# Performance work log

Measured on AMD Instinct MI355X. Metric: run time of the kernel, lower is better.

Reference implementation:

```python
import jax, jax.numpy as jnp
import numpy as np

N_EMBD = 1024
N_HEAD = 16
B, T = 4, 2048
EPS = 1e-5


def setup_inputs() -> dict:
    key = jax.random.key(0)
    ks = jax.random.split(key, 12)
    s = 0.02
    d, dff = N_EMBD, 4 * N_EMBD
    return {
        "x": jax.random.normal(ks[0], (B, T, d), dtype=jnp.float32),
        "ln1_w": jnp.ones((d,), jnp.float32),
        "ln1_b": jnp.zeros((d,), jnp.float32),
        "ln2_w": jnp.ones((d,), jnp.float32),
        "ln2_b": jnp.zeros((d,), jnp.float32),
        "w_attn": jax.random.normal(ks[1], (d, 3 * d), jnp.float32) * s,
        "b_attn": jnp.zeros((3 * d,), jnp.float32),
        "w_proj": jax.random.normal(ks[2], (d, d), jnp.float32) * s,
        "b_proj": jnp.zeros((d,), jnp.float32),
        "w_fc": jax.random.normal(ks[3], (d, dff), jnp.float32) * s,
        "b_fc": jnp.zeros((dff,), jnp.float32),
        "w_fc2": jax.random.normal(ks[4], (dff, d), jnp.float32) * s,
        "b_fc2": jnp.zeros((d,), jnp.float32),
    }


def _layernorm(x, w, b):
    mu = jnp.mean(x, axis=-1, keepdims=True)
    var = jnp.mean(jnp.square(x - mu), axis=-1, keepdims=True)
    return (x - mu) * jax.lax.rsqrt(var + EPS) * w + b


def reference(x, ln1_w, ln1_b, ln2_w, ln2_b, w_attn, b_attn, w_proj, b_proj,
              w_fc, b_fc, w_fc2, b_fc2):
    Bx, Tx, C = x.shape
    hd = C // N_HEAD
    # --- attention branch ---
    h = _layernorm(x, ln1_w, ln1_b)
    qkv = h @ w_attn + b_attn  # [B,T,3C]
    q, k, v = jnp.split(qkv, 3, axis=-1)
    q = q.reshape(Bx, Tx, N_HEAD, hd).transpose(0, 2, 1, 3)  # [B,H,T,hd]
    k = k.reshape(Bx, Tx, N_HEAD, hd).transpose(0, 2, 1, 3)
    v = v.reshape(Bx, Tx, N_HEAD, hd).transpose(0, 2, 1, 3)
    att = jnp.einsum("bhqd,bhkd->bhqk", q, k) * (1.0 / np.sqrt(hd))
    causal = jnp.tril(jnp.ones((Tx, Tx), dtype=bool))
    att = jnp.where(causal[None, None], att, -jnp.inf)
    att = jax.nn.softmax(att, axis=-1)
    y = jnp.einsum("bhqk,bhkd->bhqd", att, v)
    y = y.transpose(0, 2, 1, 3).reshape(Bx, Tx, C)
    x = x + (y @ w_proj + b_proj)
    # --- mlp branch ---
    h2 = _layernorm(x, ln2_w, ln2_b)
    m = jax.nn.gelu(h2 @ w_fc + b_fc, approximate=False)
    x = x + (m @ w_fc2 + b_fc2)
    return x
```

## Files before the change

### kernel.cpp

```cpp
#include <hip/hip_runtime.h>
#include <hip/hip_bf16.h>
#include <math.h>

typedef __bf16 bf16;
typedef __bf16 bf16x8 __attribute__((ext_vector_type(8)));
typedef float f32x4 __attribute__((ext_vector_type(4)));

__device__ __forceinline__ void gload_lds16(const bf16* g, bf16* l) {
  __builtin_amdgcn_global_load_lds(
      (const __attribute__((address_space(1))) void*)g,
      (__attribute__((address_space(3))) void*)l, 16, 0, 0);
}

#define MF(a, b, c) __builtin_amdgcn_mfma_f32_16x16x32_bf16((a), (b), (c), 0, 0, 0)
#define VM4_BAR()  asm volatile("s_waitcnt vmcnt(4)\ns_barrier" ::: "memory")
#define VM2_BAR()  asm volatile("s_waitcnt vmcnt(2)\ns_barrier" ::: "memory")
#define VM0_BAR()  asm volatile("s_waitcnt vmcnt(0)\ns_barrier" ::: "memory")
#define BAR_ONLY() asm volatile("s_barrier" ::: "memory")
#define LGK0_SB()  do { asm volatile("s_waitcnt lgkmcnt(0)" ::: "memory"); \
                        __builtin_amdgcn_sched_barrier(0); } while (0)

template <int EPI, int KSPLIT>
__global__ __launch_bounds__(512, 2)
void gemmq(const bf16* __restrict__ A, const bf16* __restrict__ BT,
           const float* __restrict__ bias, const float* __restrict__ res,
           void* __restrict__ Cout, void* __restrict__ Cout2,
           int M, int N, int K)
{
  __shared__ alignas(16) bf16 lsA[2][16384];
  __shared__ alignas(16) bf16 lsB[2][16384];

  int nbn = N >> 8;
  int nwg = (M >> 8) * nbn;
  int bid = blockIdx.x;
  int ks = 0;
  if (KSPLIT == 2) { ks = (bid >= nwg) ? 1 : 0; bid -= ks * nwg; }
  int cpx = nwg >> 3;
  int wg  = (bid & 7) * cpx + (bid >> 3);
  int m0 = (wg / nbn) << 8;
  int n0 = (wg % nbn) << 8;

  int t = threadIdx.x;
  int l = t & 63, w = t >> 6;
  int wr = (w >> 2) << 6;
  int wc = (w & 3) << 5;
  int lr = l & 15, lg = l >> 4;

  int kb0 = (KSPLIT == 2) ? ks * (K >> 1) : 0;
  int nt = (K / KSPLIT) >> 6;

  const bf16* Ag = A  + (size_t)m0 * K + kb0;
  const bf16* Bg = BT + (size_t)n0 * K + kb0;

  int swz0 = (lg ^ (lr & 7)) << 3;
  int swz1 = swz0 ^ 32;
  int aRow = (wr + lr) << 6;
  int bRow = (wc + lr) << 6;

  const bf16* srcA[2]; const bf16* srcB[2];
#pragma unroll
  for (int j = 0; j < 2; ++j) {
    int ci = j * 512 + t;
    int r = ci >> 3;
    int g = (ci & 7) ^ (r & 7);
    srcA[j] = Ag + (size_t)r * K + g * 8;
    srcB[j] = Bg + (size_t)r * K + g * 8;
  }
  size_t qA = (size_t)128 * K;

#define STAGE_A(q, kofs, db) do { \
  _Pragma("unroll") \
  for (int j = 0; j < 2; ++j) \
    gload_lds16(srcA[j] + (q) * qA + (kofs), &lsA[db][(q) * 8192 + (j * 512 + t) * 8]); \
} while (0)
#define STAGE_B(q, kofs, db) do { \
  _Pragma("unroll") \
  for (int j = 0; j < 2; ++j) \
    gload_lds16(srcB[j] + (q) * qA + (kofs), &lsB[db][(q) * 8192 + (j * 512 + t) * 8]); \
} while (0)

  f32x4 acc[2][2][4][2];
  f32x4 zero = {0.f, 0.f, 0.f, 0.f};
#pragma unroll
  for (int qa = 0; qa < 2; ++qa)
#pragma unroll
    for (int qb = 0; qb < 2; ++qb)
#pragma unroll
      for (int mi = 0; mi < 4; ++mi)
#pragma unroll
        for (int ni = 0; ni < 2; ++ni) acc[qa][qb][mi][ni] = zero;

  STAGE_A(0, 0, 0);
  STAGE_B(0, 0, 0);
  STAGE_B(1, 0, 0);
  STAGE_A(1, 0, 0);

  bf16x8 afr[4][2], bfr[2][2];

  for (int T = 0; T < nt; ++T) {
    int c = T & 1, d = c ^ 1;
    bool st = (T + 1 < nt);
    int k64 = (T + 1) << 6;
    const bf16* pa = &lsA[c][0];
    const bf16* pb = &lsB[c][0];

    VM4_BAR();
#pragma unroll
    for (int mi = 0; mi < 4; ++mi) {
      afr[mi][0] = *(const bf16x8*)(pa + aRow + mi * 1024 + swz0);
      afr[mi][1] = *(const bf16x8*)(pa + aRow + mi * 1024 + swz1);
    }
#pragma unroll
    for (int ni = 0; ni < 2; ++ni) {
      bfr[ni][0] = *(const bf16x8*)(pb + bRow + ni * 1024 + swz0);
      bfr[ni][1] = *(const bf16x8*)(pb + bRow + ni * 1024 + swz1);
    }
    if (st) STAGE_A(0, k64, d);
    LGK0_SB();
    __builtin_amdgcn_s_setprio(1);
#pragma unroll
    for (int mi = 0; mi < 4; ++mi)
#pragma unroll
      for (int ni = 0; ni < 2; ++ni)
#pragma unroll
        for (int kk = 0; kk < 2; ++kk)
          acc[0][0][mi][ni] = MF(afr[mi][kk], bfr[ni][kk], acc[0][0][mi][ni]);
    __builtin_amdgcn_s_setprio(0);

    if (st) VM4_BAR(); else VM2_BAR();
#pragma unroll
    for (int ni = 0; ni < 2; ++ni) {
      bfr[ni][0] = *(const bf16x8*)(pb + 8192 + bRow + ni * 1024 + swz0);
      bfr[ni][1] = *(const bf16x8*)(pb + 8192 + bRow + ni * 1024 + swz1);
    }
    if (st) STAGE_B(0, k64, d);
    LGK0_SB();
    __builtin_amdgcn_s_setprio(1);
#pragma unroll
    for (int mi = 0; mi < 4; ++mi)
#pragma unroll
      for (int ni = 0; ni < 2; ++ni)
#pragma unroll
        for (int kk = 0; kk < 2; ++kk)
          acc[0][1][mi][ni] = MF(afr[mi][kk], bfr[ni][kk], acc[0][1][mi][ni]);
    __builtin_amdgcn_s_setprio(0);

    if (st) VM4_BAR(); else VM0_BAR();
#pragma unroll
    for (int mi = 0; mi < 4; ++mi) {
      afr[mi][0] = *(const bf16x8*)(pa + 8192 + aRow + mi * 1024 + swz0);
      afr[mi][1] = *(const bf16x8*)(pa + 8192 + aRow + mi * 1024 + swz1);
    }
    if (st) STAGE_B(1, k64, d);
    LGK0_SB();
    __builtin_amdgcn_s_setprio(1);
#pragma unroll
    for (int mi = 0; mi < 4; ++mi)
#pragma unroll
      for (int ni = 0; ni < 2; ++ni)
#pragma unroll
        for (int kk = 0; kk < 2; ++kk)
          acc[1][1][mi][ni] = MF(afr[mi][kk], bfr[ni][kk], acc[1][1][mi][ni]);
    __builtin_amdgcn_s_setprio(0);

    BAR_ONLY();
#pragma unroll
    for (int ni = 0; ni < 2; ++ni) {
      bfr[ni][0] = *(const bf16x8*)(pb + bRow + ni * 1024 + swz0);
      bfr[ni][1] = *(const bf16x8*)(pb + bRow + ni * 1024 + swz1);
    }
    if (st) STAGE_A(1, k64, d);
    LGK0_SB();
    __builtin_amdgcn_s_setprio(1);
#pragma unroll
    for (int mi = 0; mi < 4; ++mi)
#pragma unroll
      for (int ni = 0; ni < 2; ++ni)
#pragma unroll
        for (int kk = 0; kk < 2; ++kk)
          acc[1][0][mi][ni] = MF(afr[mi][kk], bfr[ni][kk], acc[1][0][mi][ni]);
    __builtin_amdgcn_s_setprio(0);
  }

  bf16* Pb = (bf16*)((KSPLIT == 2 && ks) ? Cout2 : Cout);
#pragma unroll
  for (int qa = 0; qa < 2; ++qa)
#pragma unroll
    for (int mi = 0; mi < 4; ++mi) {
      int row = m0 + qa * 128 + wr + mi * 16 + lg * 4;
#pragma unroll
      for (int qb = 0; qb < 2; ++qb)
#pragma unroll
        for (int ni = 0; ni < 2; ++ni) {
          int col = n0 + qb * 128 + wc + ni * 16 + lr;
          float bv = (EPI == 3) ? 0.f : bias[col];
          f32x4 a = acc[qa][qb][mi][ni];
#pragma unroll
          for (int r = 0; r < 4; ++r) {
            float v = a[r] + bv;
            size_t idx = (size_t)(row + r) * N + col;
            if (EPI == 0)      Pb[idx] = (bf16)v;
            else if (EPI == 1) ((float*)Cout)[idx] = v + res[idx];
            else if (EPI == 2) Pb[idx] = (bf16)(0.5f * v * (1.f + erff(v * 0.70710678118654752f)));
            else               Pb[idx] = (bf16)v;
          }
        }
    }
#undef STAGE_A
#undef STAGE_B
}

__global__ __launch_bounds__(256)
void combine2(const bf16* __restrict__ p0, const bf16* __restrict__ p1,
              const float* __restrict__ bias, const float* __restrict__ res,
              float* __restrict__ out)
{
  int i = (blockIdx.x * 256 + threadIdx.x) * 8;
  bf16x8 a = *(const bf16x8*)(p0 + i);
  bf16x8 b = *(const bf16x8*)(p1 + i);
  int c = i & 1023;
#pragma unroll
  for (int j = 0; j < 8; ++j)
    out[i + j] = (float)a[j] + (float)b[j] + bias[c + j] + res[i + j];
}

__global__ __launch_bounds__(256)
void ln_bf16(const float* __restrict__ x, const float* __restrict__ w,
             const float* __restrict__ b, bf16* __restrict__ out)
{
  int row = blockIdx.x;
  int t = threadIdx.x;
  float4 v = ((const float4*)(x + (size_t)row * 1024))[t];
  float s  = v.x + v.y + v.z + v.w;
  float sq = v.x * v.x + v.y * v.y + v.z * v.z + v.w * v.w;
#pragma unroll
  for (int off = 32; off >= 1; off >>= 1) {
    s  += __shfl_xor(s, off);
    sq += __shfl_xor(sq, off);
  }
  __shared__ float ps[4], pq[4];
  if ((t & 63) == 0) { ps[t >> 6] = s; pq[t >> 6] = sq; }
  __syncthreads();
  s  = ps[0] + ps[1] + ps[2] + ps[3];
  sq = pq[0] + pq[1] + pq[2] + pq[3];
  float mu  = s * (1.f / 1024.f);
  float var = sq * (1.f / 1024.f) - mu * mu;
  float rstd = rsqrtf(var + 1e-5f);
  float4 wv = ((const float4*)w)[t];
  float4 bv = ((const float4*)b)[t];
  size_t o0 = (size_t)row * 1024 + t * 4;
  out[o0 + 0] = (bf16)((v.x - mu) * rstd * wv.x + bv.x);
  out[o0 + 1] = (bf16)((v.y - mu) * rstd * wv.y + bv.y);
  out[o0 + 2] = (bf16)((v.z - mu) * rstd * wv.z + bv.z);
  out[o0 + 3] = (bf16)((v.w - mu) * rstd * wv.w + bv.w);
}

__global__ __launch_bounds__(256)
void transpose_cast(const float* __restrict__ W, bf16* __restrict__ WT, int K, int N)
{
  __shared__ float tile[32][33];
  int bk = blockIdx.x * 32, bn = blockIdx.y * 32;
  int tx = threadIdx.x & 31, ty = threadIdx.x >> 5;
#pragma unroll
  for (int i = ty; i < 32; i += 8)
    tile[i][tx] = W[(size_t)(bk + i) * N + bn + tx];
  __syncthreads();
#pragma unroll
  for (int i = ty; i < 32; i += 8)
    WT[(size_t)(bn + i) * K + bk + tx] = (bf16)tile[tx][i];
}

__global__ __launch_bounds__(256)
void vtrans(const bf16* __restrict__ qkv, bf16* __restrict__ vt)
{
  __shared__ alignas(16) bf16 tile[64 * 64];
  int bh = blockIdx.x;
  int b = bh >> 4, h = bh & 15;
  int t0 = blockIdx.y * 64;
  int t = threadIdx.x;
#pragma unroll
  for (int i = 0; i < 2; ++i) {
    int c = i * 256 + t;
    int tt = c >> 3, d8 = c & 7;
    bf16x8 v = *(const bf16x8*)(qkv + (size_t)(b * 2048 + t0 + tt) * 3072 + 2048 + h * 64 + d8 * 8);
    *(bf16x8*)&tile[(tt * 8 + (d8 ^ (tt >> 3))) * 8] = v;
  }
  __syncthreads();
#pragma unroll
  for (int i = 0; i < 2; ++i) {
    int c = i * 256 + t;
    int d = c >> 3, tt8 = c & 7;
    bf16x8 o;
#pragma unroll
    for (int j = 0; j < 8; ++j) {
      int row = tt8 * 8 + j;
      o[j] = tile[(row * 8 + ((d >> 3) ^ (row >> 3))) * 8 + (d & 7)];
    }
    *(bf16x8*)(vt + (size_t)(bh * 64 + d) * 2048 + t0 + tt8 * 8) = o;
  }
}

__global__ __launch_bounds__(256)
void attn_flash(const bf16* __restrict__ qkv, const bf16* __restrict__ vt,
                bf16* __restrict__ y)
{
  __shared__ alignas(16) bf16 lk[64 * 64];
  __shared__ alignas(16) bf16 lv[64 * 64];
  __shared__ alignas(16) bf16 lp[4][16 * 64];

  int bid = blockIdx.x;
  int bh = bid & 63;
  int qb = 31 - (bid >> 6);
  int b = bh >> 4, h = bh & 15;
  int t = threadIdx.x;
  int w = t >> 6, l = t & 63;
  int lr = l & 15, lg = l >> 4;
  int q0 = qb * 64;
  int qw = q0 + w * 16;
  const size_t RS = 3072;
  const float SCL = 0.18033688011112042f;

  const bf16* qbase = qkv + (size_t)(b * 2048) * RS + h * 64;
  const bf16* kbase = qkv + (size_t)(b * 2048) * RS + 1024 + h * 64;
  const bf16* vtb   = vt + (size_t)(bh * 64) * 2048;

  bf16x8 qf[2];
#pragma unroll
  for (int kk = 0; kk < 2; ++kk)
    qf[kk] = *(const bf16x8*)(qbase + (size_t)(qw + lr) * RS + kk * 32 + lg * 8);

  f32x4 zero = {0.f, 0.f, 0.f, 0.f};
  f32x4 o[4];
#pragma unroll
  for (int ni = 0; ni < 4; ++ni) o[ni] = zero;
  float lo[4] = {0.f, 0.f, 0.f, 0.f};

  int nkb = qb + 1;
  for (int kb = 0; kb < nkb; ++kb) {
    int k0 = kb * 64;
#pragma unroll
    for (int i = 0; i < 2; ++i) {
      int c = i * 256 + t;
      int row = c >> 3, c8 = c & 7;
      int sc8 = c8 ^ (row & 7);
      gload_lds16(kbase + (size_t)(k0 + row) * RS + sc8 * 8, &lk[c * 8]);
      gload_lds16(vtb + (size_t)row * 2048 + k0 + sc8 * 8, &lv[c * 8]);
    }
    __syncthreads();

    f32x4 s[4];
#pragma unroll
    for (int j = 0; j < 4; ++j) s[j] = zero;
#pragma unroll
    for (int kk = 0; kk < 2; ++kk)
#pragma unroll
      for (int j = 0; j < 4; ++j) {
        int krow = j * 16 + lr;
        bf16x8 kf = *(const bf16x8*)&lk[krow * 64 + (((4 * kk + lg) ^ (krow & 7)) * 8)];
        s[j] = MF(qf[kk], kf, s[j]);
      }

    bool needmask = (kb == qb);
    float p[4][4];
#pragma unroll
    for (int r = 0; r < 4; ++r) {
      int tq = qw + lg * 4 + r;
#pragma unroll
      for (int j = 0; j < 4; ++j) {
        float v = s[j][r] * SCL;
        if (needmask && (k0 + j * 16 + lr > tq)) v = -1e30f;
        p[j][r] = exp2f(v);
      }
      lo[r] += (p[0][r] + p[1][r]) + (p[2][r] + p[3][r]);
    }

#pragma unroll
    for (int r = 0; r < 4; ++r) {
      int qr = lg * 4 + r;
#pragma unroll
      for (int j = 0; j < 4; ++j) {
        int ch = (2 * j + (lr >> 3)) ^ (qr & 7);
        lp[w][qr * 64 + ch * 8 + (lr & 7)] = (bf16)p[j][r];
      }
    }
    bf16x8 pa[2];
#pragma unroll
    for (int kf = 0; kf < 2; ++kf)
      pa[kf] = *(const bf16x8*)&lp[w][lr * 64 + (((4 * kf + lg) ^ (lr & 7)) * 8)];

#pragma unroll
    for (int ni = 0; ni < 4; ++ni)
#pragma unroll
      for (int kf = 0; kf < 2; ++kf) {
        int d = ni * 16 + lr;
        bf16x8 vf = *(const bf16x8*)&lv[d * 64 + (((4 * kf + lg) ^ (d & 7)) * 8)];
        o[ni] = MF(pa[kf], vf, o[ni]);
      }
    __syncthreads();
  }

#pragma unroll
  for (int r = 0; r < 4; ++r) {
#pragma unroll
    for (int off = 1; off < 16; off <<= 1) lo[r] += __shfl_xor(lo[r], off);
    lo[r] = 1.f / lo[r];
  }
#pragma unroll
  for (int ni = 0; ni < 4; ++ni)
#pragma unroll
    for (int r = 0; r < 4; ++r) {
      int tq = qw + lg * 4 + r;
      y[(size_t)(b * 2048 + tq) * 1024 + h * 64 + ni * 16 + lr] = (bf16)(o[ni][r] * lo[r]);
    }
}

extern "C" void kernel_launch(void* const* d_in, const int* in_sizes, int n_in,
                              void* d_out, int out_size, void* d_ws, size_t ws_size,
                              hipStream_t stream) {
  (void)in_sizes; (void)n_in; (void)out_size; (void)ws_size;
  const float* x      = (const float*)d_in[0];
  const float* ln1w   = (const float*)d_in[1];
  const float* ln1b   = (const float*)d_in[2];
  const float* ln2w   = (const float*)d_in[3];
  const float* ln2b   = (const float*)d_in[4];
  const float* w_attn = (const float*)d_in[5];
  const float* b_attn = (const float*)d_in[6];
  const float* w_proj = (const float*)d_in[7];
  const float* b_proj = (const float*)d_in[8];
  const float* w_fc   = (const float*)d_in[9];
  const float* b_fc   = (const float*)d_in[10];
  const float* w_fc2  = (const float*)d_in[11];
  const float* b_fc2  = (const float*)d_in[12];
  float* out = (float*)d_out;

  char* p = (char*)d_ws;
  bf16*  h     = (bf16*)p;  p += (size_t)8192 * 1024 * 2;
  bf16*  qkv   = (bf16*)p;
  bf16*  mbuf  = (bf16*)p;  p += (size_t)8192 * 3072 * 2;
  bf16*  ybuf  = (bf16*)p;  p += (size_t)8192 * 1024 * 2;
  float* x1    = (float*)p; p += (size_t)8192 * 1024 * 4;
  bf16*  wqkvT = (bf16*)p;  p += (size_t)3072 * 1024 * 2;
  bf16*  wprojT= (bf16*)p;  p += (size_t)1024 * 1024 * 2;
  bf16*  wfcT  = (bf16*)p;  p += (size_t)4096 * 1024 * 2;
  bf16*  wfc2T = (bf16*)p;  p += (size_t)1024 * 4096 * 2;
  bf16*  vt    = (bf16*)x1;
  bf16*  pp0   = qkv;
  bf16*  pp1   = qkv + (size_t)8192 * 1024;
  bf16*  sp0   = h;
  bf16*  sp1   = wqkvT;

  transpose_cast<<<dim3(1024 / 32, 3072 / 32), 256, 0, stream>>>(w_attn, wqkvT, 1024, 3072);
  transpose_cast<<<dim3(1024 / 32, 1024 / 32), 256, 0, stream>>>(w_proj, wprojT, 1024, 1024);
  transpose_cast<<<dim3(1024 / 32, 4096 / 32), 256, 0, stream>>>(w_fc,   wfcT,  1024, 4096);
  transpose_cast<<<dim3(4096 / 32, 1024 / 32), 256, 0, stream>>>(w_fc2,  wfc2T, 4096, 1024);

  ln_bf16<<<8192, 256, 0, stream>>>(x, ln1w, ln1b, h);
  gemmq<0, 1><<<384, 512, 0, stream>>>(h, wqkvT, b_attn, nullptr, qkv, nullptr, 8192, 3072, 1024);
  vtrans<<<dim3(64, 32), 256, 0, stream>>>(qkv, vt);
  attn_flash<<<2048, 256, 0, stream>>>(qkv, vt, ybuf);
  gemmq<3, 2><<<256, 512, 0, stream>>>(ybuf, wprojT, nullptr, nullptr, pp0, pp1, 8192, 1024, 1024);
  combine2<<<4096, 256, 0, stream>>>(pp0, pp1, b_proj, x, x1);
  ln_bf16<<<8192, 256, 0, stream>>>(x1, ln2w, ln2b, h);
  gemmq<2, 1><<<512, 512, 0, stream>>>(h, wfcT, b_fc, nullptr, mbuf, nullptr, 8192, 4096, 1024);
  gemmq<3, 2><<<256, 512, 0, stream>>>(mbuf, wfc2T, nullptr, nullptr, sp0, sp1, 8192, 1024, 4096);
  combine2<<<4096, 256, 0, stream>>>(sp0, sp1, b_fc2, x1, out);
}
```

Measured before the change: 439.1 us.

## Double-buffer attention K/V, fuse combine with LN2, keep B fragments in registers

```diff
diff --git a/kernel.cpp b/kernel.cpp
--- a/kernel.cpp
+++ b/kernel.cpp
@@ -3,6 +3,7 @@
 #include <math.h>
 
 typedef __bf16 bf16;
+typedef __bf16 bf16x4 __attribute__((ext_vector_type(4)));
 typedef __bf16 bf16x8 __attribute__((ext_vector_type(8)));
 typedef float f32x4 __attribute__((ext_vector_type(4)));
 
@@ -16,7 +17,6 @@
 #define VM4_BAR()  asm volatile("s_waitcnt vmcnt(4)\ns_barrier" ::: "memory")
 #define VM2_BAR()  asm volatile("s_waitcnt vmcnt(2)\ns_barrier" ::: "memory")
 #define VM0_BAR()  asm volatile("s_waitcnt vmcnt(0)\ns_barrier" ::: "memory")
-#define BAR_ONLY() asm volatile("s_barrier" ::: "memory")
 #define LGK0_SB()  do { asm volatile("s_waitcnt lgkmcnt(0)" ::: "memory"); \
                         __builtin_amdgcn_sched_barrier(0); } while (0)
 
@@ -95,7 +95,7 @@
   STAGE_B(1, 0, 0);
   STAGE_A(1, 0, 0);
 
-  bf16x8 afr[4][2], bfr[2][2];
+  bf16x8 afr[4][2], bfr0[2][2], bfr1[2][2];
 
   for (int T = 0; T < nt; ++T) {
     int c = T & 1, d = c ^ 1;
@@ -112,8 +112,8 @@
     }
 #pragma unroll
     for (int ni = 0; ni < 2; ++ni) {
-      bfr[ni][0] = *(const bf16x8*)(pb + bRow + ni * 1024 + swz0);
-      bfr[ni][1] = *(const bf16x8*)(pb + bRow + ni * 1024 + swz1);
+      bfr0[ni][0] = *(const bf16x8*)(pb + bRow + ni * 1024 + swz0);
+      bfr0[ni][1] = *(const bf16x8*)(pb + bRow + ni * 1024 + swz1);
     }
     if (st) STAGE_A(0, k64, d);
     LGK0_SB();
@@ -124,14 +124,14 @@
       for (int ni = 0; ni < 2; ++ni)
 #pragma unroll
         for (int kk = 0; kk < 2; ++kk)
-          acc[0][0][mi][ni] = MF(afr[mi][kk], bfr[ni][kk], acc[0][0][mi][ni]);
+          acc[0][0][mi][ni] = MF(afr[mi][kk], bfr0[ni][kk], acc[0][0][mi][ni]);
     __builtin_amdgcn_s_setprio(0);
 
     if (st) VM4_BAR(); else VM2_BAR();
 #pragma unroll
     for (int ni = 0; ni < 2; ++ni) {
-      bfr[ni][0] = *(const bf16x8*)(pb + 8192 + bRow + ni * 1024 + swz0);
-      bfr[ni][1] = *(const bf16x8*)(pb + 8192 + bRow + ni * 1024 + swz1);
+      bfr1[ni][0] = *(const bf16x8*)(pb + 8192 + bRow + ni * 1024 + swz0);
+      bfr1[ni][1] = *(const bf16x8*)(pb + 8192 + bRow + ni * 1024 + swz1);
     }
     if (st) STAGE_B(0, k64, d);
     LGK0_SB();
@@ -142,7 +142,7 @@
       for (int ni = 0; ni < 2; ++ni)
 #pragma unroll
         for (int kk = 0; kk < 2; ++kk)
-          acc[0][1][mi][ni] = MF(afr[mi][kk], bfr[ni][kk], acc[0][1][mi][ni]);
+          acc[0][1][mi][ni] = MF(afr[mi][kk], bfr1[ni][kk], acc[0][1][mi][ni]);
     __builtin_amdgcn_s_setprio(0);
 
     if (st) VM4_BAR(); else VM0_BAR();
@@ -160,17 +160,10 @@
       for (int ni = 0; ni < 2; ++ni)
 #pragma unroll
         for (int kk = 0; kk < 2; ++kk)
-          acc[1][1][mi][ni] = MF(afr[mi][kk], bfr[ni][kk], acc[1][1][mi][ni]);
+          acc[1][1][mi][ni] = MF(afr[mi][kk], bfr1[ni][kk], acc[1][1][mi][ni]);
     __builtin_amdgcn_s_setprio(0);
 
-    BAR_ONLY();
-#pragma unroll
-    for (int ni = 0; ni < 2; ++ni) {
-      bfr[ni][0] = *(const bf16x8*)(pb + bRow + ni * 1024 + swz0);
-      bfr[ni][1] = *(const bf16x8*)(pb + bRow + ni * 1024 + swz1);
-    }
     if (st) STAGE_A(1, k64, d);
-    LGK0_SB();
     __builtin_amdgcn_s_setprio(1);
 #pragma unroll
     for (int mi = 0; mi < 4; ++mi)
@@ -178,7 +171,7 @@
       for (int ni = 0; ni < 2; ++ni)
 #pragma unroll
         for (int kk = 0; kk < 2; ++kk)
-          acc[1][0][mi][ni] = MF(afr[mi][kk], bfr[ni][kk], acc[1][0][mi][ni]);
+          acc[1][0][mi][ni] = MF(afr[mi][kk], bfr0[ni][kk], acc[1][0][mi][ni]);
     __builtin_amdgcn_s_setprio(0);
   }
 
@@ -222,6 +215,48 @@
 #pragma unroll
   for (int j = 0; j < 8; ++j)
     out[i + j] = (float)a[j] + (float)b[j] + bias[c + j] + res[i + j];
+}
+
+__global__ __launch_bounds__(256)
+void combine_ln(const bf16* __restrict__ p0, const bf16* __restrict__ p1,
+                const float* __restrict__ bias, const float* __restrict__ res,
+                const float* __restrict__ lnw, const float* __restrict__ lnb,
+                float* __restrict__ x1, bf16* __restrict__ hout)
+{
+  int row = blockIdx.x;
+  int t = threadIdx.x;
+  size_t i0 = (size_t)row * 1024 + t * 4;
+  bf16x4 a = *(const bf16x4*)(p0 + i0);
+  bf16x4 b = *(const bf16x4*)(p1 + i0);
+  float4 r = *(const float4*)(res + i0);
+  float4 bi = ((const float4*)bias)[t];
+  float v0 = (float)a[0] + (float)b[0] + bi.x + r.x;
+  float v1 = (float)a[1] + (float)b[1] + bi.y + r.y;
+  float v2 = (float)a[2] + (float)b[2] + bi.z + r.z;
+  float v3 = (float)a[3] + (float)b[3] + bi.w + r.w;
+  float4 vv = {v0, v1, v2, v3};
+  *(float4*)(x1 + i0) = vv;
+  float s  = v0 + v1 + v2 + v3;
+  float sq = v0 * v0 + v1 * v1 + v2 * v2 + v3 * v3;
+#pragma unroll
+  for (int off = 32; off >= 1; off >>= 1) {
+    s  += __shfl_xor(s, off);
+    sq += __shfl_xor(sq, off);
+  }
+  __shared__ float ps[4], pq[4];
+  if ((t & 63) == 0) { ps[t >> 6] = s; pq[t >> 6] = sq; }
+  __syncthreads();
+  s  = ps[0] + ps[1] + ps[2] + ps[3];
+  sq = pq[0] + pq[1] + pq[2] + pq[3];
+  float mu  = s * (1.f / 1024.f);
+  float var = sq * (1.f / 1024.f) - mu * mu;
+  float rstd = rsqrtf(var + 1e-5f);
+  float4 wv = ((const float4*)lnw)[t];
+  float4 bv = ((const float4*)lnb)[t];
+  hout[i0 + 0] = (bf16)((v0 - mu) * rstd * wv.x + bv.x);
+  hout[i0 + 1] = (bf16)((v1 - mu) * rstd * wv.y + bv.y);
+  hout[i0 + 2] = (bf16)((v2 - mu) * rstd * wv.z + bv.z);
+  hout[i0 + 3] = (bf16)((v3 - mu) * rstd * wv.w + bv.w);
 }
 
 __global__ __launch_bounds__(256)
@@ -304,8 +339,8 @@
 void attn_flash(const bf16* __restrict__ qkv, const bf16* __restrict__ vt,
                 bf16* __restrict__ y)
 {
-  __shared__ alignas(16) bf16 lk[64 * 64];
-  __shared__ alignas(16) bf16 lv[64 * 64];
+  __shared__ alignas(16) bf16 lk[2][4096];
+  __shared__ alignas(16) bf16 lv[2][4096];
   __shared__ alignas(16) bf16 lp[4][16 * 64];
 
   int bid = blockIdx.x;
@@ -329,6 +364,17 @@
   for (int kk = 0; kk < 2; ++kk)
     qf[kk] = *(const bf16x8*)(qbase + (size_t)(qw + lr) * RS + kk * 32 + lg * 8);
 
+  const bf16* pK[2]; const bf16* pV[2]; int dst[2];
+#pragma unroll
+  for (int i = 0; i < 2; ++i) {
+    int c = i * 256 + t;
+    int row = c >> 3, c8 = c & 7;
+    int sc8 = c8 ^ (row & 7);
+    pK[i] = kbase + (size_t)row * RS + sc8 * 8;
+    pV[i] = vtb + (size_t)row * 2048 + sc8 * 8;
+    dst[i] = c * 8;
+  }
+
   f32x4 zero = {0.f, 0.f, 0.f, 0.f};
   f32x4 o[4];
 #pragma unroll
@@ -336,17 +382,25 @@
   float lo[4] = {0.f, 0.f, 0.f, 0.f};
 
   int nkb = qb + 1;
+#pragma unroll
+  for (int i = 0; i < 2; ++i) {
+    gload_lds16(pK[i], &lk[0][dst[i]]);
+    gload_lds16(pV[i], &lv[0][dst[i]]);
+  }
+
   for (int kb = 0; kb < nkb; ++kb) {
+    int cur = kb & 1;
     int k0 = kb * 64;
-#pragma unroll
-    for (int i = 0; i < 2; ++i) {
-      int c = i * 256 + t;
-      int row = c >> 3, c8 = c & 7;
-      int sc8 = c8 ^ (row & 7);
-      gload_lds16(kbase + (size_t)(k0 + row) * RS + sc8 * 8, &lk[c * 8]);
-      gload_lds16(vtb + (size_t)row * 2048 + k0 + sc8 * 8, &lv[c * 8]);
-    }
-    __syncthreads();
+    VM0_BAR();
+    if (kb + 1 < nkb) {
+#pragma unroll
+      for (int i = 0; i < 2; ++i) {
+        pK[i] += 64 * RS;
+        pV[i] += 64;
+        gload_lds16(pK[i], &lk[cur ^ 1][dst[i]]);
+        gload_lds16(pV[i], &lv[cur ^ 1][dst[i]]);
+      }
+    }
 
     f32x4 s[4];
 #pragma unroll
@@ -356,7 +410,7 @@
 #pragma unroll
       for (int j = 0; j < 4; ++j) {
         int krow = j * 16 + lr;
-        bf16x8 kf = *(const bf16x8*)&lk[krow * 64 + (((4 * kk + lg) ^ (krow & 7)) * 8)];
+        bf16x8 kf = *(const bf16x8*)&lk[cur][krow * 64 + (((4 * kk + lg) ^ (krow & 7)) * 8)];
         s[j] = MF(qf[kk], kf, s[j]);
       }
 
@@ -393,10 +447,9 @@
 #pragma unroll
       for (int kf = 0; kf < 2; ++kf) {
         int d = ni * 16 + lr;
-        bf16x8 vf = *(const bf16x8*)&lv[d * 64 + (((4 * kf + lg) ^ (d & 7)) * 8)];
+        bf16x8 vf = *(const bf16x8*)&lv[cur][d * 64 + (((4 * kf + lg) ^ (d & 7)) * 8)];
         o[ni] = MF(pa[kf], vf, o[ni]);
       }
-    __syncthreads();
   }
 
 #pragma unroll
@@ -459,8 +512,7 @@
   vtrans<<<dim3(64, 32), 256, 0, stream>>>(qkv, vt);
   attn_flash<<<2048, 256, 0, stream>>>(qkv, vt, ybuf);
   gemmq<3, 2><<<256, 512, 0, stream>>>(ybuf, wprojT, nullptr, nullptr, pp0, pp1, 8192, 1024, 1024);
-  combine2<<<4096, 256, 0, stream>>>(pp0, pp1, b_proj, x, x1);
-  ln_bf16<<<8192, 256, 0, stream>>>(x1, ln2w, ln2b, h);
+  combine_ln<<<8192, 256, 0, stream>>>(pp0, pp1, b_proj, x, ln2w, ln2b, x1, h);
   gemmq<2, 1><<<512, 512, 0, stream>>>(h, wfcT, b_fc, nullptr, mbuf, nullptr, 8192, 4096, 1024);
   gemmq<3, 2><<<256, 512, 0, stream>>>(mbuf, wfc2T, nullptr, nullptr, sp0, sp1, 8192, 1024, 4096);
   combine2<<<4096, 256, 0, stream>>>(sp0, sp1, b_fc2, x1, out);
```

New measurement: 409.5 us. 6.7% less time.
